# Performance work log

Measured on AMD Instinct MI355X. Metric: run time of the kernel, lower is better.

The kernel has to match this reference:

```python
import jax, jax.numpy as jnp
import numpy as np

D_MODEL = 512
NUM_HEADS = 8
NUM_LAYERS = 4
SEQ_LEN = 2048
BATCH = 2
LN_EPS = 1e-5


def _layer_norm(x, g, b):
    mu = jnp.mean(x, axis=-1, keepdims=True)
    var = jnp.mean(jnp.square(x - mu), axis=-1, keepdims=True)
    return (x - mu) * jax.lax.rsqrt(var + LN_EPS) * g + b


def setup_inputs() -> dict:
    key = jax.random.key(0)
    ks = jax.random.split(key, 12)
    d, nl = D_MODEL, NUM_LAYERS
    s = 0.02
    return {
        "x": jax.random.normal(ks[0], (BATCH, SEQ_LEN, d), dtype=jnp.float32),
        "mask": jnp.zeros((1, 1, SEQ_LEN, SEQ_LEN), dtype=jnp.float32),
        "Wqkv": jax.random.normal(ks[1], (nl, d, 3 * d), dtype=jnp.float32) * s,
        "Wout": jax.random.normal(ks[2], (nl, d, d), dtype=jnp.float32) * s,
        "ln_g": jnp.ones((nl, d), dtype=jnp.float32),
        "ln_b": jnp.zeros((nl, d), dtype=jnp.float32),
        "W1": jax.random.normal(ks[3], (nl, d, 4 * d), dtype=jnp.float32) * s,
        "b1": jnp.zeros((nl, 4 * d), dtype=jnp.float32),
        "alpha": jnp.full((nl,), 0.01, dtype=jnp.float32),  # PReLU(init=0.01), scalar per block
        "W2": jax.random.normal(ks[4], (nl, 4 * d, d), dtype=jnp.float32) * s,
        "b2": jnp.zeros((nl, d), dtype=jnp.float32),
        "lnf_g": jnp.ones((d,), dtype=jnp.float32),
        "lnf_b": jnp.zeros((d,), dtype=jnp.float32),
    }


def _encoder(x, mask, Wqkv, Wout, ln_g, ln_b, W1, b1, alpha, W2, b2, lnf_g, lnf_b):
    B, L, d = x.shape
    H = NUM_HEADS
    dh = d // H
    scale = 1.0 / (d ** 0.5)  # NOTE: scales by sqrt(d_model), not head dim (as in source)

    def block(x, p):
        wqkv, wout, g, b, w1, b1_, a, w2, b2_ = p
        qkv = x @ wqkv  # [B, L, 3d]
        q, k, v = jnp.split(qkv, 3, axis=-1)
        # b l (h j) -> b h l j
        to_heads = lambda t: t.reshape(B, L, H, dh).transpose(0, 2, 1, 3)
        q, k, v = to_heads(q) * scale, to_heads(k), to_heads(v)
        e = jnp.einsum('bhlj,bhkj->bhlk', q, k) + mask  # [B, H, L, L]
        att = jnp.nan_to_num(jax.nn.softmax(e, axis=-1))
        # Faithful to source: repeated index takes the DIAGONAL of att,
        # then multiplies elementwise into v (NOT a matmul).
        out = jnp.einsum('bhll,bhlj->bhlj', att, v)
        out = out.transpose(0, 2, 1, 3).reshape(B, L, d)  # b h l j -> b l (h j)
        out = out @ wout
        out_att = _layer_norm(out + x, g, b)
        h = out_att @ w1 + b1_
        h = jnp.where(h >= 0, h, a * h)  # PReLU (dropout=0 in eval)
        h = h @ w2 + b2_
        # same LayerNorm params reused (same nn.LayerNorm instance in source)
        return _layer_norm(h + out_att, g, b), None

    params = (Wqkv, Wout, ln_g, ln_b, W1, b1, alpha, W2, b2)
    x, _ = jax.lax.scan(block, x, params)
    return _layer_norm(x, lnf_g, lnf_b)


def reference(x, mask, Wqkv, Wout, ln_g, ln_b, W1, b1, alpha, W2, b2, lnf_g, lnf_b):
    return _encoder(x, mask, Wqkv, Wout, ln_g, ln_b, W1, b1, alpha, W2, b2, lnf_g, lnf_b)
```

## Files before the change

kernel.cpp:

```cpp
#include <hip/hip_runtime.h>
#include <math.h>

typedef unsigned short u16;
typedef __attribute__((ext_vector_type(8))) short short8;
typedef __attribute__((ext_vector_type(4))) float f32x4;

#define SEQ 2048
#define NHEADS 8
#define NLAYERS 4
#define NROWS 4096
#define SCALE_QK_LOG2E 0.06376571201f
#define PART_STRIDE ((size_t)NROWS * 512)

#define GLOAD_LDS(gp, lp) __builtin_amdgcn_global_load_lds( \
    (const __attribute__((address_space(1))) uint4*)(gp), \
    (__attribute__((address_space(3))) uint4*)(lp), 16, 0, 0)

__device__ __forceinline__ float b2f(u16 u){
    union { unsigned int i; float f; } c; c.i = ((unsigned int)u) << 16; return c.f;
}
__device__ __forceinline__ u16 f2b(float f){
    union { float f; unsigned int i; } c; c.f = f;
    unsigned int x = c.i;
    unsigned int r = x + 0x7fffu + ((x >> 16) & 1u);
    return (u16)(r >> 16);
}
__device__ __forceinline__ void unpack8(uint4 u, float* f){
    f[0]=b2f(u.x & 0xffffu); f[1]=b2f(u.x >> 16);
    f[2]=b2f(u.y & 0xffffu); f[3]=b2f(u.y >> 16);
    f[4]=b2f(u.z & 0xffffu); f[5]=b2f(u.z >> 16);
    f[6]=b2f(u.w & 0xffffu); f[7]=b2f(u.w >> 16);
}
__device__ __forceinline__ uint4 pack8(const float* f){
    uint4 u;
    u.x = (unsigned)f2b(f[0]) | ((unsigned)f2b(f[1]) << 16);
    u.y = (unsigned)f2b(f[2]) | ((unsigned)f2b(f[3]) << 16);
    u.z = (unsigned)f2b(f[4]) | ((unsigned)f2b(f[5]) << 16);
    u.w = (unsigned)f2b(f[6]) | ((unsigned)f2b(f[7]) << 16);
    return u;
}

__global__ __launch_bounds__(256)
void cvt_f32_bf16(const float* __restrict__ in, u16* __restrict__ out, int n8){
    int i = blockIdx.x * 256 + threadIdx.x;
    if (i >= n8) return;
    const float4* p = (const float4*)(in + (size_t)i * 8);
    float4 a = p[0], b = p[1];
    float f[8] = {a.x, a.y, a.z, a.w, b.x, b.y, b.z, b.w};
    *((uint4*)(out + (size_t)i * 8)) = pack8(f);
}

__global__ __launch_bounds__(256)
void transpose_all(const float* __restrict__ Wqkv, const float* __restrict__ Wout,
                   const float* __restrict__ W1,  const float* __restrict__ W2,
                   u16* __restrict__ qkvT, u16* __restrict__ woutT,
                   u16* __restrict__ w1T,  u16* __restrict__ w2T)
{
    __shared__ float tile[32][33];
    int l = blockIdx.x / 3072;
    int tid = blockIdx.x % 3072;
    const float* src; u16* dst; int R, C, local;
    if (tid < 768)       { src = Wqkv + (size_t)l * 512 * 1536; dst = qkvT + (size_t)l * 1536 * 512; R = 512;  C = 1536; local = tid; }
    else if (tid < 1024) { src = Wout + (size_t)l * 512 * 512;  dst = woutT + (size_t)l * 512 * 512; R = 512;  C = 512;  local = tid - 768; }
    else if (tid < 2048) { src = W1 + (size_t)l * 512 * 2048;   dst = w1T + (size_t)l * 2048 * 512;  R = 512;  C = 2048; local = tid - 1024; }
    else                 { src = W2 + (size_t)l * 2048 * 512;   dst = w2T + (size_t)l * 512 * 2048;  R = 2048; C = 512;  local = tid - 2048; }
    int ctiles = C >> 5;
    int c0 = (local % ctiles) * 32, r0 = (local / ctiles) * 32;
    int tx = threadIdx.x & 31, ty = threadIdx.x >> 5;
#pragma unroll
    for (int i = 0; i < 4; i++){
        int r = r0 + ty + i * 8;
        tile[ty + i * 8][tx] = src[(size_t)r * C + c0 + tx];
    }
    __syncthreads();
#pragma unroll
    for (int i = 0; i < 4; i++){
        int c = c0 + ty + i * 8;
        dst[(size_t)c * R + r0 + tx] = f2b(tile[tx][ty + i * 8]);
    }
}

template<int BM, int BN, int SPLITS>
__global__ __launch_bounds__(256)
void gemm3(const u16* __restrict__ A, const u16* __restrict__ Bt,
           u16* __restrict__ C,
           const float* __restrict__ bias, const float* __restrict__ alphap,
           int N, int K)
{
    constexpr int NBY = NROWS / BM;
    constexpr int WAVES_M = BM / 64;
    constexpr int WAVES_N = 4 / WAVES_M;
    constexpr int WN = BN / WAVES_N;
    constexpr int MT = 4, NT = WN / 16;
    __shared__ __align__(16) u16 As[BM * 64];
    __shared__ __align__(16) u16 Bs[BN * 64];

    const int t = threadIdx.x;
    const int wave = t >> 6, lane = t & 63;
    const int quad = lane >> 4, l16 = lane & 15;
    const int wm = (WAVES_M == 2) ? (wave >> 1) : 0;
    const int wn = (WAVES_M == 2) ? (wave & 1) : wave;
    const int id = blockIdx.x;
    const int m0 = (id % NBY) * BM;
    const int n0 = (id / NBY) * BN;
    const int lr = lane >> 3;
    const int lc = (lane & 7) << 3;
    const int Ks = K / SPLITS;
    const int kbeg = blockIdx.z * Ks;

    f32x4 acc[MT][NT];
#pragma unroll
    for (int i = 0; i < MT; i++)
#pragma unroll
        for (int j = 0; j < NT; j++) acc[i][j] = (f32x4){0.f, 0.f, 0.f, 0.f};

    for (int kt = kbeg; kt < kbeg + Ks; kt += 64){
        __syncthreads();
#pragma unroll
        for (int j = 0; j < BM / 32; j++){
            int r0 = wave * 8 + j * 32;
            GLOAD_LDS(A + (size_t)(m0 + r0 + lr) * K + kt + lc, As + r0 * 64);
        }
#pragma unroll
        for (int j = 0; j < BN / 32; j++){
            int r0 = wave * 8 + j * 32;
            GLOAD_LDS(Bt + (size_t)(n0 + r0 + lr) * K + kt + lc, Bs + r0 * 64);
        }
        __syncthreads();
#pragma unroll
        for (int ks = 0; ks < 2; ks++){
            short8 af[MT], bf[NT];
#pragma unroll
            for (int mt = 0; mt < MT; mt++)
                af[mt] = *((const short8*)&As[(wm * 64 + mt * 16 + l16) * 64 + ks * 32 + quad * 8]);
#pragma unroll
            for (int nt = 0; nt < NT; nt++)
                bf[nt] = *((const short8*)&Bs[(wn * WN + nt * 16 + l16) * 64 + ks * 32 + quad * 8]);
#pragma unroll
            for (int mt = 0; mt < MT; mt++)
#pragma unroll
                for (int nt = 0; nt < NT; nt++)
                    acc[mt][nt] = __builtin_amdgcn_mfma_f32_16x16x32_bf16(af[mt], bf[nt], acc[mt][nt], 0, 0, 0);
        }
    }

    u16* Cp = (SPLITS > 1) ? (C + (size_t)blockIdx.z * PART_STRIDE) : C;
    const float aval = alphap ? alphap[0] : 0.f;
#pragma unroll
    for (int nt = 0; nt < NT; nt++){
        int col = n0 + wn * WN + nt * 16 + l16;
        float bv = (SPLITS == 1 && bias) ? bias[col] : 0.f;
#pragma unroll
        for (int mt = 0; mt < MT; mt++){
#pragma unroll
            for (int r = 0; r < 4; r++){
                int row = m0 + wm * 64 + mt * 16 + quad * 4 + r;
                float v = acc[mt][nt][r] + bv;
                if (SPLITS == 1 && alphap) v = (v >= 0.f) ? v : aval * v;
                Cp[(size_t)row * N + col] = f2b(v);
            }
        }
    }
}

__global__ __launch_bounds__(256)
void gemm_wout_ln(const u16* __restrict__ A, const u16* __restrict__ Bt,
                  const u16* __restrict__ res,
                  const float* __restrict__ gg, const float* __restrict__ bb,
                  u16* __restrict__ outb)
{
    constexpr int KT = 8;
    __shared__ __align__(16) u16 Bs[2][512 * 64];
    __shared__ __align__(16) u16 As[2][16 * 64];
    __shared__ float red[2][4][16];

    const int t = threadIdx.x, wave = t >> 6, lane = t & 63;
    const int quad = lane >> 4, l16 = lane & 15;
    const int lr = lane >> 3, lc = (lane & 7) << 3;
    const int m0 = blockIdx.x * 16;

    f32x4 acc[8];
#pragma unroll
    for (int nt = 0; nt < 8; nt++) acc[nt] = (f32x4){0.f, 0.f, 0.f, 0.f};

    auto STAGE = [&](int buf, int kt){
#pragma unroll
        for (int j = 0; j < 16; j++){
            int r0 = wave * 8 + j * 32;
            GLOAD_LDS(Bt + (size_t)(r0 + lr) * 512 + kt + lc, &Bs[buf][r0 * 64]);
        }
        if (wave < 2){
            int r0 = wave * 8;
            GLOAD_LDS(A + (size_t)(m0 + r0 + lr) * 512 + kt + lc, &As[buf][r0 * 64]);
        }
    };

    STAGE(0, 0);
    __syncthreads();
    for (int kt = 0; kt < KT; kt++){
        const int cur = kt & 1;
        if (kt + 1 < KT) STAGE(cur ^ 1, (kt + 1) * 64);
#pragma unroll
        for (int ks = 0; ks < 2; ks++){
            short8 af = *((const short8*)&As[cur][l16 * 64 + ks * 32 + quad * 8]);
            short8 bf[8];
#pragma unroll
            for (int nt = 0; nt < 8; nt++)
                bf[nt] = *((const short8*)&Bs[cur][(wave * 128 + nt * 16 + l16) * 64 + ks * 32 + quad * 8]);
#pragma unroll
            for (int nt = 0; nt < 8; nt++)
                acc[nt] = __builtin_amdgcn_mfma_f32_16x16x32_bf16(af, bf[nt], acc[nt], 0, 0, 0);
        }
        __syncthreads();
    }

    float vv[8][4];
    float s0[4] = {0.f, 0.f, 0.f, 0.f};
    float s1[4] = {0.f, 0.f, 0.f, 0.f};
#pragma unroll
    for (int nt = 0; nt < 8; nt++){
        int col = wave * 128 + nt * 16 + l16;
#pragma unroll
        for (int r = 0; r < 4; r++){
            int row = quad * 4 + r;
            float val = acc[nt][r] + b2f(res[(size_t)(m0 + row) * 512 + col]);
            vv[nt][r] = val;
            s0[r] += val;
            s1[r] += val * val;
        }
    }
#pragma unroll
    for (int off = 1; off < 16; off <<= 1){
#pragma unroll
        for (int r = 0; r < 4; r++){
            s0[r] += __shfl_xor(s0[r], off, 64);
            s1[r] += __shfl_xor(s1[r], off, 64);
        }
    }
    if (l16 == 0){
#pragma unroll
        for (int r = 0; r < 4; r++){
            red[0][wave][quad * 4 + r] = s0[r];
            red[1][wave][quad * 4 + r] = s1[r];
        }
    }
    __syncthreads();
    float mu[4], rsd[4];
#pragma unroll
    for (int r = 0; r < 4; r++){
        int row = quad * 4 + r;
        float S = red[0][0][row] + red[0][1][row] + red[0][2][row] + red[0][3][row];
        float Q = red[1][0][row] + red[1][1][row] + red[1][2][row] + red[1][3][row];
        float m = S * (1.f / 512.f);
        float var = Q * (1.f / 512.f) - m * m;
        mu[r] = m;
        rsd[r] = rsqrtf(var + 1e-5f);
    }
#pragma unroll
    for (int nt = 0; nt < 8; nt++){
        int col = wave * 128 + nt * 16 + l16;
        float g = gg[col], b = bb[col];
#pragma unroll
        for (int r = 0; r < 4; r++){
            int row = quad * 4 + r;
            float o = (vv[nt][r] - mu[r]) * rsd[r] * g + b;
            outb[(size_t)(m0 + row) * 512 + col] = f2b(o);
        }
    }
}

__global__ __launch_bounds__(256)
void attn_scores2(const u16* __restrict__ qkv, float* __restrict__ rowsum_parts)
{
    __shared__ __align__(16) u16 Qs[128 * 64];
    __shared__ __align__(16) u16 Ks[128 * 64];
    const int t = threadIdx.x, wave = t >> 6, lane = t & 63;
    const int quad = lane >> 4, l16 = lane & 15;
    const int wm = wave >> 1, wn = wave & 1;
    const int id = blockIdx.x;
    const int bh = id & 15, ly = (id >> 4) & 15, ksp = id >> 8;
    const int b = bh >> 3, h = bh & 7;
    const int lr = lane >> 3, lc = (lane & 7) << 3;
    const size_t qbase = (size_t)(b * SEQ + ly * 128) * 1536 + h * 64;

#pragma unroll
    for (int j = 0; j < 4; j++){
        int r0 = wave * 8 + j * 32;
        GLOAD_LDS(qkv + qbase + (size_t)(r0 + lr) * 1536 + lc, Qs + r0 * 64);
    }

    float rs[4][4];
#pragma unroll
    for (int i = 0; i < 4; i++)
#pragma unroll
        for (int j = 0; j < 4; j++) rs[i][j] = 0.f;

    for (int kxi = 0; kxi < 4; kxi++){
        const int kx = ksp * 4 + kxi;
        const size_t kbase = (size_t)(b * SEQ + kx * 128) * 1536 + 512 + h * 64;
        __syncthreads();
#pragma unroll
        for (int j = 0; j < 4; j++){
            int r0 = wave * 8 + j * 32;
            GLOAD_LDS(qkv + kbase + (size_t)(r0 + lr) * 1536 + lc, Ks + r0 * 64);
        }
        __syncthreads();

        f32x4 acc[4][4];
#pragma unroll
        for (int i = 0; i < 4; i++)
#pragma unroll
            for (int j = 0; j < 4; j++) acc[i][j] = (f32x4){0.f, 0.f, 0.f, 0.f};
#pragma unroll
        for (int ks = 0; ks < 2; ks++){
            short8 af[4], bf[4];
#pragma unroll
            for (int mt = 0; mt < 4; mt++)
                af[mt] = *((const short8*)&Qs[(wm * 64 + mt * 16 + l16) * 64 + ks * 32 + quad * 8]);
#pragma unroll
            for (int nt = 0; nt < 4; nt++)
                bf[nt] = *((const short8*)&Ks[(wn * 64 + nt * 16 + l16) * 64 + ks * 32 + quad * 8]);
#pragma unroll
            for (int mt = 0; mt < 4; mt++)
#pragma unroll
                for (int nt = 0; nt < 4; nt++)
                    acc[mt][nt] = __builtin_amdgcn_mfma_f32_16x16x32_bf16(af[mt], bf[nt], acc[mt][nt], 0, 0, 0);
        }
#pragma unroll
        for (int mt = 0; mt < 4; mt++)
#pragma unroll
            for (int nt = 0; nt < 4; nt++)
#pragma unroll
                for (int r = 0; r < 4; r++)
                    rs[mt][r] += exp2f(acc[mt][nt][r] * SCALE_QK_LOG2E);
    }

#pragma unroll
    for (int off = 1; off < 16; off <<= 1){
#pragma unroll
        for (int mt = 0; mt < 4; mt++)
#pragma unroll
            for (int r = 0; r < 4; r++)
                rs[mt][r] += __shfl_xor(rs[mt][r], off, 64);
    }
    if (l16 == 0){
        const int part = ksp * 2 + wn;
        float* dst = rowsum_parts + (size_t)part * 16 * SEQ + (size_t)bh * SEQ + ly * 128;
#pragma unroll
        for (int mt = 0; mt < 4; mt++)
#pragma unroll
            for (int r = 0; r < 4; r++)
                dst[wm * 64 + mt * 16 + quad * 4 + r] = rs[mt][r];
    }
}

__global__ __launch_bounds__(256)
void attn_scale(const u16* __restrict__ qkv, const float* __restrict__ rowsum_parts,
                u16* __restrict__ attnb)
{
    int gid = blockIdx.x * 256 + threadIdx.x;
    int row = gid >> 6;
    int col = (gid & 63) << 3;
    int head = col >> 6;
    int b = row >> 11, l = row & 2047;
    size_t base = (size_t)row * 1536 + col;

    float qv[8], kv[8];
    unpack8(*((const uint4*)(qkv + base)), qv);
    unpack8(*((const uint4*)(qkv + base + 512)), kv);
    float dot = 0.f;
#pragma unroll
    for (int j = 0; j < 8; j++) dot += qv[j] * kv[j];
#pragma unroll
    for (int off = 1; off < 8; off <<= 1) dot += __shfl_xor(dot, off, 64);

    size_t idx = (size_t)(b * 8 + head) * SEQ + l;
    float rsum = 0.f;
#pragma unroll
    for (int p = 0; p < 8; p++) rsum += rowsum_parts[(size_t)p * 16 * SEQ + idx];
    float a = exp2f(dot * SCALE_QK_LOG2E) / rsum;

    float f[8];
    unpack8(*((const uint4*)(qkv + base + 1024)), f);
#pragma unroll
    for (int j = 0; j < 8; j++) f[j] *= a;
    *((uint4*)(attnb + (size_t)row * 512 + col)) = pack8(f);
}

__global__ __launch_bounds__(256)
void ln_kernel(const u16* __restrict__ res, int nparts,
               const float* __restrict__ bias, const u16* __restrict__ xin,
               const float* __restrict__ gg, const float* __restrict__ bb,
               u16* __restrict__ outb, float* __restrict__ outf)
{
    const int row = blockIdx.x * 4 + (threadIdx.x >> 6);
    const int lane = threadIdx.x & 63;
    const size_t base = (size_t)row * 512 + lane * 8;

    float v[8];
    unpack8(*((const uint4*)(xin + base)), v);
    for (int p = 0; p < nparts; p++){
        float rv[8];
        unpack8(*((const uint4*)(res + (size_t)p * PART_STRIDE + base)), rv);
#pragma unroll
        for (int j = 0; j < 8; j++) v[j] += rv[j];
    }
    if (bias){
        const float4* bp4 = (const float4*)(bias + lane * 8);
        float4 c0 = bp4[0], c1 = bp4[1];
        v[0] += c0.x; v[1] += c0.y; v[2] += c0.z; v[3] += c0.w;
        v[4] += c1.x; v[5] += c1.y; v[6] += c1.z; v[7] += c1.w;
    }
    float s = 0.f;
#pragma unroll
    for (int j = 0; j < 8; j++) s += v[j];
#pragma unroll
    for (int off = 32; off; off >>= 1) s += __shfl_xor(s, off, 64);
    float mu = s * (1.f / 512.f);
    float q = 0.f;
#pragma unroll
    for (int j = 0; j < 8; j++){ float d = v[j] - mu; q += d * d; }
#pragma unroll
    for (int off = 32; off; off >>= 1) q += __shfl_xor(q, off, 64);
    float rs = rsqrtf(q * (1.f / 512.f) + 1e-5f);

    const float4* gp = (const float4*)(gg + lane * 8);
    const float4* bp = (const float4*)(bb + lane * 8);
    float4 g0 = gp[0], g1 = gp[1], bb0 = bp[0], bb1 = bp[1];
    float gv[8] = {g0.x, g0.y, g0.z, g0.w, g1.x, g1.y, g1.z, g1.w};
    float bv[8] = {bb0.x, bb0.y, bb0.z, bb0.w, bb1.x, bb1.y, bb1.z, bb1.w};
    float o[8];
#pragma unroll
    for (int j = 0; j < 8; j++) o[j] = (v[j] - mu) * rs * gv[j] + bv[j];
    if (outb){
        *((uint4*)(outb + base)) = pack8(o);
    } else {
        float4* op = (float4*)(outf + base);
        op[0] = make_float4(o[0], o[1], o[2], o[3]);
        op[1] = make_float4(o[4], o[5], o[6], o[7]);
    }
}

extern "C" void kernel_launch(void* const* d_in, const int* in_sizes, int n_in,
                              void* d_out, int out_size, void* d_ws, size_t ws_size,
                              hipStream_t stream)
{
    const float* x_in  = (const float*)d_in[0];
    const float* Wqkv  = (const float*)d_in[2];
    const float* Wout  = (const float*)d_in[3];
    const float* ln_g  = (const float*)d_in[4];
    const float* ln_b  = (const float*)d_in[5];
    const float* W1    = (const float*)d_in[6];
    const float* b1    = (const float*)d_in[7];
    const float* alpha = (const float*)d_in[8];
    const float* W2    = (const float*)d_in[9];
    const float* b2    = (const float*)d_in[10];
    const float* lnf_g = (const float*)d_in[11];
    const float* lnf_b = (const float*)d_in[12];
    float* out = (float*)d_out;

    char* w = (char*)d_ws;
    u16* qkvT  = (u16*)w;  w += (size_t)NLAYERS * 1536 * 512 * 2;
    u16* woutT = (u16*)w;  w += (size_t)NLAYERS * 512 * 512 * 2;
    u16* w1T   = (u16*)w;  w += (size_t)NLAYERS * 2048 * 512 * 2;
    u16* w2T   = (u16*)w;  w += (size_t)NLAYERS * 512 * 2048 * 2;
    u16* big    = (u16*)w;  w += (size_t)NROWS * 2048 * 2;
    u16* x_cur  = (u16*)w;  w += (size_t)NROWS * 512 * 2;
    u16* attnb  = (u16*)w;  w += (size_t)NROWS * 512 * 2;
    u16* outatt = (u16*)w;  w += (size_t)NROWS * 512 * 2;
    u16* tmpb   = (u16*)w;  w += (size_t)4 * PART_STRIDE * 2;
    float* rowsum_parts = (float*)w; w += (size_t)8 * 2 * NHEADS * SEQ * 4;

    u16* qkvb = big;
    u16* hbuf = big;

    cvt_f32_bf16<<<NROWS * 512 / 8 / 256, 256, 0, stream>>>(x_in, x_cur, NROWS * 512 / 8);
    transpose_all<<<NLAYERS * 3072, 256, 0, stream>>>(Wqkv, Wout, W1, W2, qkvT, woutT, w1T, w2T);

    for (int l = 0; l < NLAYERS; l++){
        const u16* wq  = qkvT  + (size_t)l * 1536 * 512;
        const u16* wo  = woutT + (size_t)l * 512 * 512;
        const u16* wf1 = w1T   + (size_t)l * 2048 * 512;
        const u16* wf2 = w2T   + (size_t)l * 512 * 2048;

        gemm3<128, 64, 1><<<dim3(24 * 32), 256, 0, stream>>>(
            x_cur, wq, qkvb, nullptr, nullptr, 1536, 512);

        attn_scores2<<<1024, 256, 0, stream>>>(qkvb, rowsum_parts);
        attn_scale<<<NROWS * 512 / 8 / 256, 256, 0, stream>>>(qkvb, rowsum_parts, attnb);

        gemm_wout_ln<<<256, 256, 0, stream>>>(attnb, wo, x_cur,
            ln_g + l * 512, ln_b + l * 512, outatt);

        gemm3<128, 128, 1><<<dim3(16 * 32), 256, 0, stream>>>(
            outatt, wf1, hbuf, b1 + (size_t)l * 2048, alpha + l, 2048, 512);

        gemm3<64, 128, 2><<<dim3(4 * 64, 1, 2), 256, 0, stream>>>(
            hbuf, wf2, tmpb, nullptr, nullptr, 512, 2048);

        ln_kernel<<<NROWS / 4, 256, 0, stream>>>(tmpb, 2, b2 + (size_t)l * 512, outatt,
            ln_g + l * 512, ln_b + l * 512, x_cur, nullptr);
    }

    ln_kernel<<<NROWS / 4, 256, 0, stream>>>(nullptr, 0, nullptr, x_cur, lnf_g, lnf_b, nullptr, out);
}
```

Baseline: 536.4 us.

## Fuse attention diagonal scaling into Wout GEMM prologue; raise FFN2 split-K to 4

The separate attn_scale kernel goes away. Each gemm_wout_ln block now computes the diagonal softmax weight times V for its 16 rows and writes the result straight into LDS as the full A tile, which removes one launch and the attnb global round trip. The W2 GEMM split-K also goes from 2 to 4 partitions, with ln_kernel summing 4 partials. In exchange there is more LDS per block for the Wout kernel and more partial-sum traffic for the W2 path.

```diff
diff --git a/kernel.cpp b/kernel.cpp
--- a/kernel.cpp
+++ b/kernel.cpp
@@ -164,14 +164,14 @@
 }
 
 __global__ __launch_bounds__(256)
-void gemm_wout_ln(const u16* __restrict__ A, const u16* __restrict__ Bt,
-                  const u16* __restrict__ res,
+void gemm_wout_ln(const u16* __restrict__ qkv, const float* __restrict__ rowsum_parts,
+                  const u16* __restrict__ Bt, const u16* __restrict__ res,
                   const float* __restrict__ gg, const float* __restrict__ bb,
                   u16* __restrict__ outb)
 {
     constexpr int KT = 8;
     __shared__ __align__(16) u16 Bs[2][512 * 64];
-    __shared__ __align__(16) u16 As[2][16 * 64];
+    __shared__ __align__(16) u16 As[16 * 512];
     __shared__ float red[2][4][16];
 
     const int t = threadIdx.x, wave = t >> 6, lane = t & 63;
@@ -179,30 +179,55 @@
     const int lr = lane >> 3, lc = (lane & 7) << 3;
     const int m0 = blockIdx.x * 16;
 
-    f32x4 acc[8];
-#pragma unroll
-    for (int nt = 0; nt < 8; nt++) acc[nt] = (f32x4){0.f, 0.f, 0.f, 0.f};
-
-    auto STAGE = [&](int buf, int kt){
+    auto STAGE_B = [&](int buf, int kt){
 #pragma unroll
         for (int j = 0; j < 16; j++){
             int r0 = wave * 8 + j * 32;
             GLOAD_LDS(Bt + (size_t)(r0 + lr) * 512 + kt + lc, &Bs[buf][r0 * 64]);
         }
-        if (wave < 2){
-            int r0 = wave * 8;
-            GLOAD_LDS(A + (size_t)(m0 + r0 + lr) * 512 + kt + lc, &As[buf][r0 * 64]);
-        }
     };
 
-    STAGE(0, 0);
+    STAGE_B(0, 0);
+
+#pragma unroll
+    for (int it = 0; it < 4; it++){
+        int rl = it * 4 + wave;
+        int row = m0 + rl;
+        int col = lane << 3;
+        int head = col >> 6;
+        size_t base = (size_t)row * 1536 + col;
+        float qv[8], kv[8];
+        unpack8(*((const uint4*)(qkv + base)), qv);
+        unpack8(*((const uint4*)(qkv + base + 512)), kv);
+        float dot = 0.f;
+#pragma unroll
+        for (int j = 0; j < 8; j++) dot += qv[j] * kv[j];
+#pragma unroll
+        for (int off = 1; off < 8; off <<= 1) dot += __shfl_xor(dot, off, 64);
+        int b = row >> 11, l = row & 2047;
+        size_t idx = (size_t)(b * 8 + head) * SEQ + l;
+        float rsum = 0.f;
+#pragma unroll
+        for (int p = 0; p < 8; p++) rsum += rowsum_parts[(size_t)p * 16 * SEQ + idx];
+        float a = exp2f(dot * SCALE_QK_LOG2E) / rsum;
+        float f[8];
+        unpack8(*((const uint4*)(qkv + base + 1024)), f);
+#pragma unroll
+        for (int j = 0; j < 8; j++) f[j] *= a;
+        *((uint4*)&As[rl * 512 + col]) = pack8(f);
+    }
+
+    f32x4 acc[8];
+#pragma unroll
+    for (int nt = 0; nt < 8; nt++) acc[nt] = (f32x4){0.f, 0.f, 0.f, 0.f};
+
     __syncthreads();
     for (int kt = 0; kt < KT; kt++){
         const int cur = kt & 1;
-        if (kt + 1 < KT) STAGE(cur ^ 1, (kt + 1) * 64);
+        if (kt + 1 < KT) STAGE_B(cur ^ 1, (kt + 1) * 64);
 #pragma unroll
         for (int ks = 0; ks < 2; ks++){
-            short8 af = *((const short8*)&As[cur][l16 * 64 + ks * 32 + quad * 8]);
+            short8 af = *((const short8*)&As[l16 * 512 + kt * 64 + ks * 32 + quad * 8]);
             short8 bf[8];
 #pragma unroll
             for (int nt = 0; nt < 8; nt++)
@@ -352,39 +377,6 @@
             for (int r = 0; r < 4; r++)
                 dst[wm * 64 + mt * 16 + quad * 4 + r] = rs[mt][r];
     }
-}
-
-__global__ __launch_bounds__(256)
-void attn_scale(const u16* __restrict__ qkv, const float* __restrict__ rowsum_parts,
-                u16* __restrict__ attnb)
-{
-    int gid = blockIdx.x * 256 + threadIdx.x;
-    int row = gid >> 6;
-    int col = (gid & 63) << 3;
-    int head = col >> 6;
-    int b = row >> 11, l = row & 2047;
-    size_t base = (size_t)row * 1536 + col;
-
-    float qv[8], kv[8];
-    unpack8(*((const uint4*)(qkv + base)), qv);
-    unpack8(*((const uint4*)(qkv + base + 512)), kv);
-    float dot = 0.f;
-#pragma unroll
-    for (int j = 0; j < 8; j++) dot += qv[j] * kv[j];
-#pragma unroll
-    for (int off = 1; off < 8; off <<= 1) dot += __shfl_xor(dot, off, 64);
-
-    size_t idx = (size_t)(b * 8 + head) * SEQ + l;
-    float rsum = 0.f;
-#pragma unroll
-    for (int p = 0; p < 8; p++) rsum += rowsum_parts[(size_t)p * 16 * SEQ + idx];
-    float a = exp2f(dot * SCALE_QK_LOG2E) / rsum;
-
-    float f[8];
-    unpack8(*((const uint4*)(qkv + base + 1024)), f);
-#pragma unroll
-    for (int j = 0; j < 8; j++) f[j] *= a;
-    *((uint4*)(attnb + (size_t)row * 512 + col)) = pack8(f);
 }
 
 __global__ __launch_bounds__(256)
@@ -466,7 +458,6 @@
     u16* w2T   = (u16*)w;  w += (size_t)NLAYERS * 512 * 2048 * 2;
     u16* big    = (u16*)w;  w += (size_t)NROWS * 2048 * 2;
     u16* x_cur  = (u16*)w;  w += (size_t)NROWS * 512 * 2;
-    u16* attnb  = (u16*)w;  w += (size_t)NROWS * 512 * 2;
     u16* outatt = (u16*)w;  w += (size_t)NROWS * 512 * 2;
     u16* tmpb   = (u16*)w;  w += (size_t)4 * PART_STRIDE * 2;
     float* rowsum_parts = (float*)w; w += (size_t)8 * 2 * NHEADS * SEQ * 4;
@@ -487,18 +478,17 @@
             x_cur, wq, qkvb, nullptr, nullptr, 1536, 512);
 
         attn_scores2<<<1024, 256, 0, stream>>>(qkvb, rowsum_parts);
-        attn_scale<<<NROWS * 512 / 8 / 256, 256, 0, stream>>>(qkvb, rowsum_parts, attnb);
-
-        gemm_wout_ln<<<256, 256, 0, stream>>>(attnb, wo, x_cur,
+
+        gemm_wout_ln<<<256, 256, 0, stream>>>(qkvb, rowsum_parts, wo, x_cur,
             ln_g + l * 512, ln_b + l * 512, outatt);
 
         gemm3<128, 128, 1><<<dim3(16 * 32), 256, 0, stream>>>(
             outatt, wf1, hbuf, b1 + (size_t)l * 2048, alpha + l, 2048, 512);
 
-        gemm3<64, 128, 2><<<dim3(4 * 64, 1, 2), 256, 0, stream>>>(
+        gemm3<64, 128, 4><<<dim3(4 * 64, 1, 4), 256, 0, stream>>>(
             hbuf, wf2, tmpb, nullptr, nullptr, 512, 2048);
 
-        ln_kernel<<<NROWS / 4, 256, 0, stream>>>(tmpb, 2, b2 + (size_t)l * 512, outatt,
+        ln_kernel<<<NROWS / 4, 256, 0, stream>>>(tmpb, 4, b2 + (size_t)l * 512, outatt,
             ln_g + l * 512, ln_b + l * 512, x_cur, nullptr);
     }
 
```

New measurement: 520.7 us. -2.9%, faster.
